# Kernel tuning notes

Hardware: AMD Instinct MI355X
Metric: run time of the kernel (lower is better)

## Reference

```python
import jax, jax.numpy as jnp
import numpy as np

B, S, D, E, K = 4, 2048, 2048, 64, 2

def setup_inputs() -> dict:
    key = jax.random.key(0)
    k1, k2, k3, k4 = jax.random.split(key, 4)
    x = jax.random.normal(k1, (B, S, D), dtype=jnp.float32)
    W = jax.random.normal(k2, (E, D), dtype=jnp.float32) * 0.02  # gate_linear.weight
    noise_weight = jax.random.normal(k3, (E,), dtype=jnp.float32) * 0.02
    noise = jax.random.normal(k4, (B, S, E), dtype=jnp.float32)  # torch.randn_like(logits), noisy_std=1.0
    return {"x": x, "W": W, "noise_weight": noise_weight, "noise": noise, "k": K}

def reference(x, W, noise_weight, noise, k):
    # logits = x @ W.T  -> [B, S, E]
    logits = jnp.einsum('bsd,ed->bse', x, W)
    # noise injection: randn * noisy_std(=1.0) * noise_weight (per-expert scale)
    logits_noisy = logits + noise * noise_weight
    # top-k over experts
    top_vals, top_idx = jax.lax.top_k(logits_noisy, k)  # [B, S, k]
    # softmax over a tensor that is -inf everywhere except the top-k slots is
    # exactly: zeros everywhere, softmax(top_vals) scattered into the top-k slots.
    probs = jax.nn.softmax(top_vals, axis=-1)  # [B, S, k]
    n_tok = B * S
    rows = jnp.arange(n_tok)[:, None]  # [n_tok, 1]
    gated = jnp.zeros((n_tok, E), dtype=logits.dtype)
    gated = gated.at[rows, top_idx.reshape(n_tok, k)].set(probs.reshape(n_tok, k))
    gated = gated.reshape(B, S, E)
    return gated, top_idx, top_vals
```

## Files before the change

### kernel.cpp

```cpp
#include <hip/hip_runtime.h>
#include <math.h>

#define NTOK 8192
#define DDIM 2048
#define NEXP 64
#define MT   16
#define PSTR 68

#define GATED_SZ (NTOK * NEXP)
#define IDX_OFF  GATED_SZ
#define VALS_OFF (GATED_SZ + NTOK * 2)

typedef _Float16 f16x8 __attribute__((ext_vector_type(8)));
typedef float    f32x4 __attribute__((ext_vector_type(4)));

static __device__ __forceinline__ void cvt_hilo(float4 v0, float4 v1,
                                                f16x8& h8, f16x8& l8)
{
    const float vv[8] = {v0.x, v0.y, v0.z, v0.w, v1.x, v1.y, v1.z, v1.w};
#pragma unroll
    for (int j = 0; j < 8; ++j) {
        const _Float16 hh = (_Float16)vv[j];
        h8[j] = hh;
        l8[j] = (_Float16)((vv[j] - (float)hh) * 4096.f);
    }
}

__global__ __launch_bounds__(512, 4) void gate_kernel(
    const float* __restrict__ x,
    const float* __restrict__ W,
    const float* __restrict__ noise_w,
    const float* __restrict__ noise,
    float* __restrict__ out)
{
    __shared__ float cbuf[8][MT * PSTR];

    const int tid  = threadIdx.x;
    const int lane = tid & 63;
    const int w    = __builtin_amdgcn_readfirstlane(tid >> 6);
    const int tokBase = blockIdx.x * MT;

    const int q = lane >> 4;
    const int m = lane & 15;

    const float* asrc = x + (size_t)(tokBase + m) * DDIM + (size_t)w * 256 + q * 8;
    const float* bsrc = W + (size_t)m * DDIM + (size_t)w * 256 + q * 8;

    f32x4 acc_hh[4], acc_lo[4];
#pragma unroll
    for (int nt = 0; nt < 4; ++nt) {
        acc_hh[nt] = (f32x4){0.f, 0.f, 0.f, 0.f};
        acc_lo[nt] = (f32x4){0.f, 0.f, 0.f, 0.f};
    }

#pragma unroll 2
    for (int s = 0; s < 8; ++s) {
        const size_t ko = (size_t)s * 32;

        const float4 a0 = *(const float4*)(asrc + ko);
        const float4 a1 = *(const float4*)(asrc + ko + 4);
        f16x8 ah, al;
        cvt_hilo(a0, a1, ah, al);

#pragma unroll
        for (int nt = 0; nt < 4; ++nt) {
            const float4 b0 = *(const float4*)(bsrc + (size_t)nt * 16 * DDIM + ko);
            const float4 b1 = *(const float4*)(bsrc + (size_t)nt * 16 * DDIM + ko + 4);
            f16x8 bh, bl;
            cvt_hilo(b0, b1, bh, bl);

            acc_hh[nt] = __builtin_amdgcn_mfma_f32_16x16x32_f16(ah, bh, acc_hh[nt], 0, 0, 0);
            acc_lo[nt] = __builtin_amdgcn_mfma_f32_16x16x32_f16(ah, bl, acc_lo[nt], 0, 0, 0);
            acc_lo[nt] = __builtin_amdgcn_mfma_f32_16x16x32_f16(al, bh, acc_lo[nt], 0, 0, 0);
        }
    }

#pragma unroll
    for (int nt = 0; nt < 4; ++nt) {
        const int e = nt * 16 + m;
#pragma unroll
        for (int r = 0; r < 4; ++r) {
            const int t = q * 4 + r;
            cbuf[w][t * PSTR + e] = acc_hh[nt][r] + acc_lo[nt][r] * (1.f / 4096.f);
        }
    }
    __syncthreads();

    const float nwv = noise_w[lane];
#pragma unroll
    for (int i = 0; i < 2; ++i) {
        const int t   = w * 2 + i;
        const int tok = tokBase + t;
        const int e   = lane;

        float v = 0.f;
#pragma unroll
        for (int p = 0; p < 8; ++p)
            v += cbuf[p][t * PSTR + e];
        v += noise[(size_t)tok * NEXP + e] * nwv;

        float m1 = v; int i1 = e;
#pragma unroll
        for (int sh = 32; sh > 0; sh >>= 1) {
            float ov = __shfl_xor(m1, sh, 64);
            int   oi = __shfl_xor(i1, sh, 64);
            if (ov > m1 || (ov == m1 && oi < i1)) { m1 = ov; i1 = oi; }
        }
        float vm = (e == i1) ? -INFINITY : v;
        float m2 = vm; int i2 = e;
#pragma unroll
        for (int sh = 32; sh > 0; sh >>= 1) {
            float ov = __shfl_xor(m2, sh, 64);
            int   oi = __shfl_xor(i2, sh, 64);
            if (ov > m2 || (ov == m2 && oi < i2)) { m2 = ov; i2 = oi; }
        }

        const float e2  = expf(m2 - m1);
        const float inv = 1.f / (1.f + e2);
        const float p1  = inv;
        const float p2  = e2 * inv;

        float gval = 0.f;
        if (e == i1) gval = p1;
        else if (e == i2) gval = p2;
        out[(size_t)tok * NEXP + e] = gval;

        if (lane == 0) {
            out[IDX_OFF  + tok * 2 + 0] = (float)i1;
            out[IDX_OFF  + tok * 2 + 1] = (float)i2;
            out[VALS_OFF + tok * 2 + 0] = m1;
            out[VALS_OFF + tok * 2 + 1] = m2;
        }
    }
}

extern "C" void kernel_launch(void* const* d_in, const int* in_sizes, int n_in,
                              void* d_out, int out_size, void* d_ws, size_t ws_size,
                              hipStream_t stream) {
    const float* x     = (const float*)d_in[0];
    const float* W     = (const float*)d_in[1];
    const float* nw    = (const float*)d_in[2];
    const float* noise = (const float*)d_in[3];
    float* out = (float*)d_out;
    (void)d_ws; (void)ws_size;

    hipLaunchKernelGGL(gate_kernel, dim3(NTOK / MT), dim3(512), 0, stream,
                       x, W, nw, noise, out);
}
```

Baseline: 131.3 us.

## Prepack W into fp16 hi/lo MFMA fragments and stage x tiles through LDS

```diff
diff --git a/kernel.cpp b/kernel.cpp
--- a/kernel.cpp
+++ b/kernel.cpp
@@ -5,14 +5,47 @@
 #define DDIM 2048
 #define NEXP 64
 #define MT   16
-#define PSTR 68
+#define ASTR 136
+#define CSTR 68
 
 #define GATED_SZ (NTOK * NEXP)
 #define IDX_OFF  GATED_SZ
 #define VALS_OFF (GATED_SZ + NTOK * 2)
 
+#define NKSTEP (DDIM / 32)
+#define NTILE  (NEXP / 16)
+#define BFRAG_HALVES ((size_t)NKSTEP * NTILE * 64 * 8)
+
 typedef _Float16 f16x8 __attribute__((ext_vector_type(8)));
 typedef float    f32x4 __attribute__((ext_vector_type(4)));
+
+__global__ void pack_b_kernel(const float* __restrict__ W,
+                              _Float16* __restrict__ Bh,
+                              _Float16* __restrict__ Bl)
+{
+    const int tid  = blockIdx.x * blockDim.x + threadIdx.x;
+    const int lane = tid & 63;
+    const int fid  = tid >> 6;
+    const int ks   = fid >> 2;
+    const int nt   = fid & 3;
+    const int e    = nt * 16 + (lane & 15);
+    const int k    = ks * 32 + (lane >> 4) * 8;
+    const float* src = W + (size_t)e * DDIM + k;
+
+    f16x8 hi, lo;
+#pragma unroll
+    for (int j = 0; j < 8; ++j) {
+        const float v = src[j];
+        const _Float16 h = (_Float16)v;
+        hi[j] = h;
+        lo[j] = (_Float16)((v - (float)h) * 4096.f);
+    }
+    *(f16x8*)(Bh + (size_t)tid * 8) = hi;
+    *(f16x8*)(Bl + (size_t)tid * 8) = lo;
+}
+
+#define BFRAG(base, ks, nt) \
+    (*(const f16x8*)((base) + ((((size_t)(ks)) * 4 + (nt)) * 64 + lane) * 8))
 
 static __device__ __forceinline__ void cvt_hilo(float4 v0, float4 v1,
                                                 f16x8& h8, f16x8& l8)
@@ -28,12 +61,13 @@
 
 __global__ __launch_bounds__(512, 4) void gate_kernel(
     const float* __restrict__ x,
-    const float* __restrict__ W,
+    const _Float16* __restrict__ Bh,
+    const _Float16* __restrict__ Bl,
     const float* __restrict__ noise_w,
     const float* __restrict__ noise,
     float* __restrict__ out)
 {
-    __shared__ float cbuf[8][MT * PSTR];
+    __shared__ _Float16 smem[8 * 2 * MT * ASTR];
 
     const int tid  = threadIdx.x;
     const int lane = tid & 63;
@@ -43,8 +77,9 @@
     const int q = lane >> 4;
     const int m = lane & 15;
 
-    const float* asrc = x + (size_t)(tokBase + m) * DDIM + (size_t)w * 256 + q * 8;
-    const float* bsrc = W + (size_t)m * DDIM + (size_t)w * 256 + q * 8;
+    _Float16* xs = smem + (size_t)w * (2 * MT * ASTR);
+
+    const float* xw = x + (size_t)tokBase * DDIM + (size_t)w * 256;
 
     f32x4 acc_hh[4], acc_lo[4];
 #pragma unroll
@@ -53,27 +88,54 @@
         acc_lo[nt] = (f32x4){0.f, 0.f, 0.f, 0.f};
     }
 
-#pragma unroll 2
-    for (int s = 0; s < 8; ++s) {
-        const size_t ko = (size_t)s * 32;
-
-        const float4 a0 = *(const float4*)(asrc + ko);
-        const float4 a1 = *(const float4*)(asrc + ko + 4);
-        f16x8 ah, al;
-        cvt_hilo(a0, a1, ah, al);
-
-#pragma unroll
-        for (int nt = 0; nt < 4; ++nt) {
-            const float4 b0 = *(const float4*)(bsrc + (size_t)nt * 16 * DDIM + ko);
-            const float4 b1 = *(const float4*)(bsrc + (size_t)nt * 16 * DDIM + ko + 4);
-            f16x8 bh, bl;
-            cvt_hilo(b0, b1, bh, bl);
-
-            acc_hh[nt] = __builtin_amdgcn_mfma_f32_16x16x32_f16(ah, bh, acc_hh[nt], 0, 0, 0);
-            acc_lo[nt] = __builtin_amdgcn_mfma_f32_16x16x32_f16(ah, bl, acc_lo[nt], 0, 0, 0);
-            acc_lo[nt] = __builtin_amdgcn_mfma_f32_16x16x32_f16(al, bh, acc_lo[nt], 0, 0, 0);
-        }
-    }
+#define LOADSUB(sc)                                                          \
+    _Pragma("unroll")                                                        \
+    for (int p = 0; p < 4; ++p) {                                            \
+        const float* src = xw + (size_t)(p * 4 + q) * DDIM + (sc) * 128 + m * 8; \
+        s0[p] = *(const float4*)(src);                                       \
+        s1[p] = *(const float4*)(src + 4);                                   \
+    }
+
+#define STAGESUB()                                                           \
+    _Pragma("unroll")                                                        \
+    for (int p = 0; p < 4; ++p) {                                            \
+        f16x8 h8, l8;                                                        \
+        cvt_hilo(s0[p], s1[p], h8, l8);                                      \
+        const int off = (p * 4 + q) * ASTR + m * 8;                          \
+        *(f16x8*)&xs[off] = h8;                                              \
+        *(f16x8*)&xs[MT * ASTR + off] = l8;                                  \
+    }
+
+#define COMPUTESUB(sc)                                                       \
+    _Pragma("unroll")                                                        \
+    for (int stp = 0; stp < 4; ++stp) {                                      \
+        const int ks = w * 8 + (sc) * 4 + stp;                               \
+        const f16x8 ah = *(const f16x8*)&xs[m * ASTR + stp * 32 + q * 8];    \
+        const f16x8 al = *(const f16x8*)&xs[MT * ASTR + m * ASTR + stp * 32 + q * 8]; \
+        _Pragma("unroll")                                                    \
+        for (int nt = 0; nt < 4; ++nt) {                                     \
+            const f16x8 bh = BFRAG(Bh, ks, nt);                              \
+            const f16x8 bl = BFRAG(Bl, ks, nt);                              \
+            acc_hh[nt] = __builtin_amdgcn_mfma_f32_16x16x32_f16(ah, bh, acc_hh[nt], 0, 0, 0); \
+            acc_lo[nt] = __builtin_amdgcn_mfma_f32_16x16x32_f16(ah, bl, acc_lo[nt], 0, 0, 0); \
+            acc_lo[nt] = __builtin_amdgcn_mfma_f32_16x16x32_f16(al, bh, acc_lo[nt], 0, 0, 0); \
+        }                                                                    \
+    }
+
+    float4 s0[4], s1[4];
+    LOADSUB(0)
+    STAGESUB()
+    LOADSUB(1)
+    COMPUTESUB(0)
+    STAGESUB()
+    COMPUTESUB(1)
+
+#undef LOADSUB
+#undef STAGESUB
+#undef COMPUTESUB
+
+    __syncthreads();
+    float* cbuf = (float*)smem;
 
 #pragma unroll
     for (int nt = 0; nt < 4; ++nt) {
@@ -81,7 +143,7 @@
 #pragma unroll
         for (int r = 0; r < 4; ++r) {
             const int t = q * 4 + r;
-            cbuf[w][t * PSTR + e] = acc_hh[nt][r] + acc_lo[nt][r] * (1.f / 4096.f);
+            cbuf[((w * MT) + t) * CSTR + e] = acc_hh[nt][r] + acc_lo[nt][r] * (1.f / 4096.f);
         }
     }
     __syncthreads();
@@ -96,7 +158,7 @@
         float v = 0.f;
 #pragma unroll
         for (int p = 0; p < 8; ++p)
-            v += cbuf[p][t * PSTR + e];
+            v += cbuf[((p * MT) + t) * CSTR + e];
         v += noise[(size_t)tok * NEXP + e] * nwv;
 
         float m1 = v; int i1 = e;
@@ -142,8 +204,12 @@
     const float* nw    = (const float*)d_in[2];
     const float* noise = (const float*)d_in[3];
     float* out = (float*)d_out;
-    (void)d_ws; (void)ws_size;
+
+    _Float16* Bh = (_Float16*)d_ws;
+    _Float16* Bl = Bh + BFRAG_HALVES;
+
+    hipLaunchKernelGGL(pack_b_kernel, dim3(64), dim3(256), 0, stream, W, Bh, Bl);
 
     hipLaunchKernelGGL(gate_kernel, dim3(NTOK / MT), dim3(512), 0, stream,
-                       x, W, nw, noise, out);
-}
+                       x, Bh, Bl, nw, noise, out);
+}
```

After: 112.0 us. 14.7% less time.
